# Optimization experiments

Hardware: AMD Instinct MI355X
Metric: run time of the kernel (lower is better)

The kernel has to match this reference:

```python
import jax, jax.numpy as jnp
import numpy as np

N = 100000       # num_nodes
E = 1600000      # num_edges (avg degree 16)
EL = 200000      # link-prediction edges
IN_C = 64
POS = 16
HID = 64
OUT = 32


def setup_inputs() -> dict:
    key = jax.random.key(0)
    ks = jax.random.split(key, 10)
    def glorot(k, shape):
        scale = 1.0 / np.sqrt(shape[0])
        return jax.random.uniform(k, shape, jnp.float32, -scale, scale)
    return {
        "x": jax.random.normal(ks[0], (N, IN_C), jnp.float32),
        "pos_emb": jax.random.normal(ks[1], (N, POS), jnp.float32),
        "W1": glorot(ks[2], (IN_C + POS, HID)),
        "b1": jnp.zeros((HID,), jnp.float32),
        "W2": glorot(ks[3], (HID, OUT)),
        "b2": jnp.zeros((OUT,), jnp.float32),
        "Wl": glorot(ks[4], (2 * OUT, 1)),
        "bl": jnp.zeros((1,), jnp.float32),
        "edge_index": jax.random.randint(ks[5], (2, E), 0, N, jnp.int32),
        "edge_label_index": jax.random.randint(ks[6], (2, EL), 0, N, jnp.int32),
    }


def reference(x, pos_emb, W1, b1, W2, b2, Wl, bl, edge_index, edge_label_index):
    n = x.shape[0]
    # GCNConv: add self-loops, symmetric deg^{-1/2} normalization (PyG defaults)
    loops = jnp.arange(n, dtype=edge_index.dtype)
    src = jnp.concatenate([edge_index[0], loops])  # [E+N]
    dst = jnp.concatenate([edge_index[1], loops])  # [E+N]
    deg = jax.ops.segment_sum(jnp.ones_like(dst, jnp.float32), dst, num_segments=n)
    dinv = jnp.where(deg > 0, jax.lax.rsqrt(jnp.maximum(deg, 1e-12)), 0.0)
    norm = dinv[src] * dinv[dst]  # [E+N]

    def gcn_conv(h, W, b):
        hw = h @ W                                    # [N, d_out] transform first
        msg = hw[src] * norm[:, None]                 # gather + normalize
        return jax.ops.segment_sum(msg, dst, num_segments=n) + b  # scatter-add

    h = jnp.concatenate([x, pos_emb], axis=1)         # [N, in+pos]
    h = jax.nn.relu(gcn_conv(h, W1, b1))              # dropout is eval no-op
    z = gcn_conv(h, W2, b2)                           # [N, out]

    s, d = edge_label_index[0], edge_label_index[1]
    zc = jnp.concatenate([z[s], z[d]], axis=1)        # [EL, 2*out]
    edge_pred = (zc @ Wl + bl)[:, 0]                  # [EL]
    return z, edge_pred
```

## Files before the change

kernel.cpp:

```cpp
#include <hip/hip_runtime.h>
#include <hip/hip_fp16.h>

#define NN 100000
#define NE 1600000
#define NEL 200000
#define TM 64
#define TM2 128

#define NBUCK 196
#define CAPB  10240
#define TPE   8192

__global__ void k_initcur(int* __restrict__ gcur) {
    int i = threadIdx.x;
    if (i < NBUCK) gcur[i] = i * CAPB;
}

__global__ __launch_bounds__(256) void k_part(const int* __restrict__ src,
                                              const int* __restrict__ dst,
                                              int* __restrict__ gcur,
                                              int* __restrict__ part) {
    __shared__ int hist[NBUCK];
    __shared__ int base[NBUCK];
    __shared__ int rk[NBUCK];
    int tid = threadIdx.x;
    for (int i = tid; i < NBUCK; i += 256) { hist[i] = 0; rk[i] = 0; }
    __syncthreads();
    int e0 = blockIdx.x * TPE;
    int e1 = min(e0 + TPE, NE);
    for (int e = e0 + tid; e < e1; e += 256)
        atomicAdd(&hist[dst[e] >> 9], 1);
    __syncthreads();
    for (int i = tid; i < NBUCK; i += 256)
        base[i] = atomicAdd(&gcur[i], hist[i]);
    __syncthreads();
    for (int e = e0 + tid; e < e1; e += 256) {
        int d = dst[e];
        int s = src[e];
        int b = d >> 9;
        int r = atomicAdd(&rk[b], 1);
        part[base[b] + r] = ((d & 511) << 17) | s;
    }
}

__global__ void k_bscan2(const int* __restrict__ gcur, int* __restrict__ bbase) {
    __shared__ int s[256];
    int t = threadIdx.x;
    int cnt = (t < NBUCK) ? (gcur[t] - t * CAPB) : 0;
    s[t] = cnt;
    __syncthreads();
    for (int st = 1; st < 256; st <<= 1) {
        int tmp = (t >= st) ? s[t - st] : 0;
        __syncthreads();
        s[t] += tmp;
        __syncthreads();
    }
    if (t < NBUCK) bbase[t] = s[t] - cnt;
}

__global__ __launch_bounds__(256) void k_build(const int* __restrict__ gcur,
                                               const int* __restrict__ bbase,
                                               const int* __restrict__ part,
                                               int* __restrict__ csr,
                                               int* __restrict__ off,
                                               float* __restrict__ dinv) {
    __shared__ int hist[512];
    __shared__ int loff[512];
    __shared__ int ssum[256];
    __shared__ int csrbuf[CAPB];
    int b = blockIdx.x;
    int tid = threadIdx.x;
    int cnt = gcur[b] - b * CAPB;
    int pbase = b * CAPB;
    int obase = bbase[b];
    hist[tid] = 0; hist[tid + 256] = 0;
    __syncthreads();
    for (int i = tid; i < cnt; i += 256)
        atomicAdd(&hist[part[pbase + i] >> 17], 1);
    __syncthreads();
    int a0 = hist[2 * tid], a1 = hist[2 * tid + 1];
    int pairs = a0 + a1;
    ssum[tid] = pairs;
    __syncthreads();
    for (int st = 1; st < 256; st <<= 1) {
        int tmp = (tid >= st) ? ssum[tid - st] : 0;
        __syncthreads();
        ssum[tid] += tmp;
        __syncthreads();
    }
    int pexcl = ssum[tid] - pairs;
    loff[2 * tid] = pexcl;
    loff[2 * tid + 1] = pexcl + a0;
    __syncthreads();
    for (int i = tid; i < 512; i += 256) {
        int d = b * 512 + i;
        if (d < NN) {
            int c = hist[i];
            off[d] = obase + loff[i] + c;
            dinv[d] = rsqrtf((float)(c + 1));
        }
    }
    hist[tid] = 0; hist[tid + 256] = 0;
    __syncthreads();
    for (int i = tid; i < cnt; i += 256) {
        int rec = part[pbase + i];
        int dl = rec >> 17;
        int r = atomicAdd(&hist[dl], 1);
        csrbuf[loff[dl] + r] = rec & 0x1FFFF;
    }
    __syncthreads();
    for (int i = tid; i < cnt; i += 256)
        csr[obase + i] = csrbuf[i];
}

__global__ __launch_bounds__(256) void k_hw1(const float* __restrict__ x,
                                             const float* __restrict__ pos,
                                             const float* __restrict__ W1,
                                             const float* __restrict__ dinv,
                                             __half* __restrict__ hw1) {
    __shared__ float sh[TM * 80];
    __shared__ float sw[80 * 64];
    int tid = threadIdx.x;
    for (int t = tid; t < 80 * 64; t += 256) sw[t] = W1[t];
    int nb = blockIdx.x * TM;
    for (int i = tid; i < TM * 64; i += 256) {
        int node = i >> 6, ch = i & 63;
        int g = nb + node;
        sh[node * 80 + ch] = (g < NN) ? x[g * 64 + ch] : 0.0f;
    }
    for (int i = tid; i < TM * 16; i += 256) {
        int node = i >> 4, ch = i & 15;
        int g = nb + node;
        sh[node * 80 + 64 + ch] = (g < NN) ? pos[g * 16 + ch] : 0.0f;
    }
    __syncthreads();
    int j  = (tid & 15) * 4;
    int nl = (tid >> 4) * 4;
    float a00=0,a01=0,a02=0,a03=0, a10=0,a11=0,a12=0,a13=0;
    float a20=0,a21=0,a22=0,a23=0, a30=0,a31=0,a32=0,a33=0;
#pragma unroll 4
    for (int k = 0; k < 80; ++k) {
        float4 wv = *(const float4*)&sw[k * 64 + j];
        float h0 = sh[(nl + 0) * 80 + k];
        float h1 = sh[(nl + 1) * 80 + k];
        float h2 = sh[(nl + 2) * 80 + k];
        float h3 = sh[(nl + 3) * 80 + k];
        a00 += h0 * wv.x; a01 += h0 * wv.y; a02 += h0 * wv.z; a03 += h0 * wv.w;
        a10 += h1 * wv.x; a11 += h1 * wv.y; a12 += h1 * wv.z; a13 += h1 * wv.w;
        a20 += h2 * wv.x; a21 += h2 * wv.y; a22 += h2 * wv.z; a23 += h2 * wv.w;
        a30 += h3 * wv.x; a31 += h3 * wv.y; a32 += h3 * wv.z; a33 += h3 * wv.w;
    }
    int g0 = nb + nl;
    union { __half2 h2v[2]; float2 f2; } u;
#define STORE_ROW(r, b0, b1, b2, b3)                                          \
    if (g0 + r < NN) {                                                        \
        float sc = dinv[g0 + r];                                              \
        u.h2v[0] = __floats2half2_rn(b0 * sc, b1 * sc);                       \
        u.h2v[1] = __floats2half2_rn(b2 * sc, b3 * sc);                       \
        *(float2*)&hw1[(g0 + r) * 64 + j] = u.f2;                             \
    }
    STORE_ROW(0, a00, a01, a02, a03)
    STORE_ROW(1, a10, a11, a12, a13)
    STORE_ROW(2, a20, a21, a22, a23)
    STORE_ROW(3, a30, a31, a32, a33)
#undef STORE_ROW
}

__global__ __launch_bounds__(256) void k_gather1(const int* __restrict__ off,
                                                 const int* __restrict__ csr,
                                                 const float* __restrict__ dinv,
                                                 const __half* __restrict__ hw,
                                                 const float* __restrict__ b1,
                                                 __half* __restrict__ h2out) {
    int lane = threadIdx.x & 63;
    int wave = threadIdx.x >> 6;
    int d = blockIdx.x * 4 + wave;
    int start = (d == 0) ? 0 : off[d - 1];
    int end = off[d];
    start = __builtin_amdgcn_readfirstlane(start);
    end   = __builtin_amdgcn_readfirstlane(end);
    float dd = dinv[d];
    float hself = __half2float(hw[d * 64 + lane]);
    float acc0 = 0.0f, acc1 = 0.0f, acc2 = 0.0f, acc3 = 0.0f;
    int e = start;
    for (; e + 7 < end; e += 8) {
        int s0 = csr[e],     s1 = csr[e + 1];
        int s2 = csr[e + 2], s3 = csr[e + 3];
        int s4 = csr[e + 4], s5 = csr[e + 5];
        int s6 = csr[e + 6], s7 = csr[e + 7];
        float g0 = __half2float(hw[s0 * 64 + lane]);
        float g1 = __half2float(hw[s1 * 64 + lane]);
        float g2 = __half2float(hw[s2 * 64 + lane]);
        float g3 = __half2float(hw[s3 * 64 + lane]);
        float g4 = __half2float(hw[s4 * 64 + lane]);
        float g5 = __half2float(hw[s5 * 64 + lane]);
        float g6 = __half2float(hw[s6 * 64 + lane]);
        float g7 = __half2float(hw[s7 * 64 + lane]);
        acc0 += g0; acc1 += g1; acc2 += g2; acc3 += g3;
        acc0 += g4; acc1 += g5; acc2 += g6; acc3 += g7;
    }
    for (; e < end; ++e)
        acc0 += __half2float(hw[csr[e] * 64 + lane]);
    float v = fmaxf(b1[lane] + dd * (((acc0 + acc1) + (acc2 + acc3)) + hself), 0.0f);
    h2out[d * 64 + lane] = __float2half_rn(v);
}

__global__ __launch_bounds__(256) void k_hw2(const __half* __restrict__ h2,
                                             const float* __restrict__ W2,
                                             const float* __restrict__ dinv,
                                             __half* __restrict__ hw2) {
    __shared__ float sh[TM2 * 65];
    __shared__ float sw[64 * 32];
    int tid = threadIdx.x;
    for (int t = tid; t < 64 * 32; t += 256) sw[t] = W2[t];
    int nb = blockIdx.x * TM2;
    for (int i = tid; i < TM2 * 64; i += 256) {
        int node = i >> 6, ch = i & 63;
        int g = nb + node;
        sh[node * 65 + ch] = (g < NN) ? __half2float(h2[g * 64 + ch]) : 0.0f;
    }
    __syncthreads();
    int j  = (tid & 7) * 4;
    int nl = (tid >> 3) * 4;
    float a00=0,a01=0,a02=0,a03=0, a10=0,a11=0,a12=0,a13=0;
    float a20=0,a21=0,a22=0,a23=0, a30=0,a31=0,a32=0,a33=0;
#pragma unroll 4
    for (int k = 0; k < 64; ++k) {
        float4 wv = *(const float4*)&sw[k * 32 + j];
        float h0 = sh[(nl + 0) * 65 + k];
        float h1 = sh[(nl + 1) * 65 + k];
        float h2v = sh[(nl + 2) * 65 + k];
        float h3 = sh[(nl + 3) * 65 + k];
        a00 += h0 * wv.x;  a01 += h0 * wv.y;  a02 += h0 * wv.z;  a03 += h0 * wv.w;
        a10 += h1 * wv.x;  a11 += h1 * wv.y;  a12 += h1 * wv.z;  a13 += h1 * wv.w;
        a20 += h2v * wv.x; a21 += h2v * wv.y; a22 += h2v * wv.z; a23 += h2v * wv.w;
        a30 += h3 * wv.x;  a31 += h3 * wv.y;  a32 += h3 * wv.z;  a33 += h3 * wv.w;
    }
    int g0 = nb + nl;
    union { __half2 h2v2[2]; float2 f2; } u;
#define STORE_ROW(r, b0, b1, b2, b3)                                          \
    if (g0 + r < NN) {                                                        \
        float sc = dinv[g0 + r];                                              \
        u.h2v2[0] = __floats2half2_rn(b0 * sc, b1 * sc);                      \
        u.h2v2[1] = __floats2half2_rn(b2 * sc, b3 * sc);                      \
        *(float2*)&hw2[(g0 + r) * 32 + j] = u.f2;                             \
    }
    STORE_ROW(0, a00, a01, a02, a03)
    STORE_ROW(1, a10, a11, a12, a13)
    STORE_ROW(2, a20, a21, a22, a23)
    STORE_ROW(3, a30, a31, a32, a33)
#undef STORE_ROW
}

__global__ __launch_bounds__(256) void k_gather2(const int* __restrict__ off,
                                                 const int* __restrict__ csr,
                                                 const float* __restrict__ dinv,
                                                 const __half* __restrict__ hw,
                                                 const float* __restrict__ b2,
                                                 float* __restrict__ outz) {
    int lane = threadIdx.x & 63;
    int half = lane >> 5;
    int j = lane & 31;
    int wave = threadIdx.x >> 6;
    int d = blockIdx.x * 4 + wave;
    int start = (d == 0) ? 0 : off[d - 1];
    int end = off[d];
    start = __builtin_amdgcn_readfirstlane(start);
    end   = __builtin_amdgcn_readfirstlane(end);
    float dd = dinv[d];
    float hself = __half2float(hw[d * 32 + j]);
    float accA = 0.0f, accB = 0.0f, accC = 0.0f, accD = 0.0f;
    int e = start;
    for (; e + 7 < end; e += 8) {
        int sA = csr[e + half];
        int sB = csr[e + half + 2];
        int sC = csr[e + half + 4];
        int sD = csr[e + half + 6];
        accA += __half2float(hw[sA * 32 + j]);
        accB += __half2float(hw[sB * 32 + j]);
        accC += __half2float(hw[sC * 32 + j]);
        accD += __half2float(hw[sD * 32 + j]);
    }
    for (int ee = e + half; ee < end; ee += 2)
        accA += __half2float(hw[csr[ee] * 32 + j]);
    float acc = (accA + accB) + (accC + accD);
    acc += __shfl(acc, lane ^ 32, 64);
    if (half == 0)
        outz[d * 32 + j] = b2[j] + dd * (acc + hself);
}

__global__ __launch_bounds__(256) void k_linkpred(const int* __restrict__ sidx,
                                                  const int* __restrict__ didx,
                                                  const float* __restrict__ z,
                                                  const float* __restrict__ Wl,
                                                  const float* __restrict__ bl,
                                                  float* __restrict__ pred) {
    int t = blockIdx.x * blockDim.x + threadIdx.x;
    int e = t >> 4;
    int l = t & 15;
    int s = sidx[e], d = didx[e];
    float2 zs = *(const float2*)&z[s * 32 + 2 * l];
    float2 zd = *(const float2*)&z[d * 32 + 2 * l];
    float2 ws = *(const float2*)&Wl[2 * l];
    float2 wd = *(const float2*)&Wl[32 + 2 * l];
    float v = zs.x * ws.x + zs.y * ws.y + zd.x * wd.x + zd.y * wd.y;
    v += __shfl_xor(v, 1, 64);
    v += __shfl_xor(v, 2, 64);
    v += __shfl_xor(v, 4, 64);
    v += __shfl_xor(v, 8, 64);
    if (l == 0) pred[e] = v + bl[0];
}

extern "C" void kernel_launch(void* const* d_in, const int* in_sizes, int n_in,
                              void* d_out, int out_size, void* d_ws, size_t ws_size,
                              hipStream_t stream) {
    const float* x    = (const float*)d_in[0];
    const float* pos  = (const float*)d_in[1];
    const float* W1   = (const float*)d_in[2];
    const float* b1   = (const float*)d_in[3];
    const float* W2   = (const float*)d_in[4];
    const float* b2   = (const float*)d_in[5];
    const float* Wl   = (const float*)d_in[6];
    const float* bl   = (const float*)d_in[7];
    const int*   ei   = (const int*)d_in[8];
    const int*   eli  = (const int*)d_in[9];
    const int* src  = ei;
    const int* dst  = ei + NE;
    const int* lsrc = eli;
    const int* ldst = eli + NEL;

    float* out_z    = (float*)d_out;
    float* out_pred = (float*)d_out + NN * 32;

    float*  dinv  = (float*)d_ws;
    int*    off   = (int*)(dinv + NN);
    int*    gcur  = off + NN;
    int*    bbase = gcur + NBUCK;
    int*    csr   = bbase + NBUCK;
    __half* hw1   = (__half*)(csr + NE);
    int*    part  = (int*)hw1;
    __half* h2    = hw1 + NN * 64;
    __half* hw2   = h2 + NN * 64;

    k_initcur<<<1, 256, 0, stream>>>(gcur);
    k_part<<<(NE + TPE - 1) / TPE, 256, 0, stream>>>(src, dst, gcur, part);
    k_bscan2<<<1, 256, 0, stream>>>(gcur, bbase);
    k_build<<<NBUCK, 256, 0, stream>>>(gcur, bbase, part, csr, off, dinv);

    k_hw1<<<(NN + TM - 1) / TM, 256, 0, stream>>>(x, pos, W1, dinv, hw1);

    k_gather1<<<NN / 4, 256, 0, stream>>>(off, csr, dinv, hw1, b1, h2);

    k_hw2<<<(NN + TM2 - 1) / TM2, 256, 0, stream>>>(h2, W2, dinv, hw2);

    k_gather2<<<NN / 4, 256, 0, stream>>>(off, csr, dinv, hw2, b2, out_z);

    k_linkpred<<<NEL * 16 / 256, 256, 0, stream>>>(lsrc, ldst, out_z, Wl, bl, out_pred);
}
```

Baseline: 309.5 us.

## Fuse second-layer transform into gather1 and merge bucket scan into build

The layer-2 weight multiply (h @ W2, scaled by dinv) now runs inside the layer-1 gather kernel. Each wave applies W2 to its freshly computed hidden row using wave shuffles and a shared-memory copy of W2, so the intermediate h2 array no longer goes to global memory and the separate k_hw2 launch is gone. On the preprocessing side, the init kernel becomes a memset and the bucket-offset scan is folded into every k_build block, removing two tiny launches. In exchange, every gather1 block loads W2 into shared memory and adds 32 shuffle-FMA steps per node, and each build block repeats a small scan.

Result: no change. 314.1 us (+1.5%).

```diff
diff --git a/kernel.cpp b/kernel.cpp
--- a/kernel.cpp
+++ b/kernel.cpp
@@ -5,16 +5,10 @@
 #define NE 1600000
 #define NEL 200000
 #define TM 64
-#define TM2 128
 
 #define NBUCK 196
 #define CAPB  10240
 #define TPE   8192
-
-__global__ void k_initcur(int* __restrict__ gcur) {
-    int i = threadIdx.x;
-    if (i < NBUCK) gcur[i] = i * CAPB;
-}
 
 __global__ __launch_bounds__(256) void k_part(const int* __restrict__ src,
                                               const int* __restrict__ dst,
@@ -32,7 +26,7 @@
         atomicAdd(&hist[dst[e] >> 9], 1);
     __syncthreads();
     for (int i = tid; i < NBUCK; i += 256)
-        base[i] = atomicAdd(&gcur[i], hist[i]);
+        base[i] = i * CAPB + atomicAdd(&gcur[i], hist[i]);
     __syncthreads();
     for (int e = e0 + tid; e < e1; e += 256) {
         int d = dst[e];
@@ -43,36 +37,29 @@
     }
 }
 
-__global__ void k_bscan2(const int* __restrict__ gcur, int* __restrict__ bbase) {
-    __shared__ int s[256];
-    int t = threadIdx.x;
-    int cnt = (t < NBUCK) ? (gcur[t] - t * CAPB) : 0;
-    s[t] = cnt;
-    __syncthreads();
-    for (int st = 1; st < 256; st <<= 1) {
-        int tmp = (t >= st) ? s[t - st] : 0;
-        __syncthreads();
-        s[t] += tmp;
-        __syncthreads();
-    }
-    if (t < NBUCK) bbase[t] = s[t] - cnt;
-}
-
 __global__ __launch_bounds__(256) void k_build(const int* __restrict__ gcur,
-                                               const int* __restrict__ bbase,
                                                const int* __restrict__ part,
                                                int* __restrict__ csr,
                                                int* __restrict__ off,
                                                float* __restrict__ dinv) {
+    __shared__ int cnts[256];
     __shared__ int hist[512];
     __shared__ int loff[512];
     __shared__ int ssum[256];
     __shared__ int csrbuf[CAPB];
     int b = blockIdx.x;
     int tid = threadIdx.x;
-    int cnt = gcur[b] - b * CAPB;
+    cnts[tid] = (tid < NBUCK) ? gcur[tid] : 0;
+    __syncthreads();
+    for (int st = 1; st < 256; st <<= 1) {
+        int tmp = (tid >= st) ? cnts[tid - st] : 0;
+        __syncthreads();
+        cnts[tid] += tmp;
+        __syncthreads();
+    }
+    int obase = (b == 0) ? 0 : cnts[b - 1];
+    int cnt = gcur[b];
     int pbase = b * CAPB;
-    int obase = bbase[b];
     hist[tid] = 0; hist[tid + 256] = 0;
     __syncthreads();
     for (int i = tid; i < cnt; i += 256)
@@ -171,7 +158,11 @@
                                                  const float* __restrict__ dinv,
                                                  const __half* __restrict__ hw,
                                                  const float* __restrict__ b1,
-                                                 __half* __restrict__ h2out) {
+                                                 const float* __restrict__ W2,
+                                                 __half* __restrict__ hw2out) {
+    __shared__ float w[64 * 32];
+    for (int t = threadIdx.x; t < 64 * 32; t += 256) w[t] = W2[t];
+    __syncthreads();
     int lane = threadIdx.x & 63;
     int wave = threadIdx.x >> 6;
     int d = blockIdx.x * 4 + wave;
@@ -202,54 +193,14 @@
     for (; e < end; ++e)
         acc0 += __half2float(hw[csr[e] * 64 + lane]);
     float v = fmaxf(b1[lane] + dd * (((acc0 + acc1) + (acc2 + acc3)) + hself), 0.0f);
-    h2out[d * 64 + lane] = __float2half_rn(v);
-}
-
-__global__ __launch_bounds__(256) void k_hw2(const __half* __restrict__ h2,
-                                             const float* __restrict__ W2,
-                                             const float* __restrict__ dinv,
-                                             __half* __restrict__ hw2) {
-    __shared__ float sh[TM2 * 65];
-    __shared__ float sw[64 * 32];
-    int tid = threadIdx.x;
-    for (int t = tid; t < 64 * 32; t += 256) sw[t] = W2[t];
-    int nb = blockIdx.x * TM2;
-    for (int i = tid; i < TM2 * 64; i += 256) {
-        int node = i >> 6, ch = i & 63;
-        int g = nb + node;
-        sh[node * 65 + ch] = (g < NN) ? __half2float(h2[g * 64 + ch]) : 0.0f;
-    }
-    __syncthreads();
-    int j  = (tid & 7) * 4;
-    int nl = (tid >> 3) * 4;
-    float a00=0,a01=0,a02=0,a03=0, a10=0,a11=0,a12=0,a13=0;
-    float a20=0,a21=0,a22=0,a23=0, a30=0,a31=0,a32=0,a33=0;
-#pragma unroll 4
-    for (int k = 0; k < 64; ++k) {
-        float4 wv = *(const float4*)&sw[k * 32 + j];
-        float h0 = sh[(nl + 0) * 65 + k];
-        float h1 = sh[(nl + 1) * 65 + k];
-        float h2v = sh[(nl + 2) * 65 + k];
-        float h3 = sh[(nl + 3) * 65 + k];
-        a00 += h0 * wv.x;  a01 += h0 * wv.y;  a02 += h0 * wv.z;  a03 += h0 * wv.w;
-        a10 += h1 * wv.x;  a11 += h1 * wv.y;  a12 += h1 * wv.z;  a13 += h1 * wv.w;
-        a20 += h2v * wv.x; a21 += h2v * wv.y; a22 += h2v * wv.z; a23 += h2v * wv.w;
-        a30 += h3 * wv.x;  a31 += h3 * wv.y;  a32 += h3 * wv.z;  a33 += h3 * wv.w;
-    }
-    int g0 = nb + nl;
-    union { __half2 h2v2[2]; float2 f2; } u;
-#define STORE_ROW(r, b0, b1, b2, b3)                                          \
-    if (g0 + r < NN) {                                                        \
-        float sc = dinv[g0 + r];                                              \
-        u.h2v2[0] = __floats2half2_rn(b0 * sc, b1 * sc);                      \
-        u.h2v2[1] = __floats2half2_rn(b2 * sc, b3 * sc);                      \
-        *(float2*)&hw2[(g0 + r) * 32 + j] = u.f2;                             \
-    }
-    STORE_ROW(0, a00, a01, a02, a03)
-    STORE_ROW(1, a10, a11, a12, a13)
-    STORE_ROW(2, a20, a21, a22, a23)
-    STORE_ROW(3, a30, a31, a32, a33)
-#undef STORE_ROW
+    int j = lane & 31;
+    int base2 = (lane >> 5) << 5;
+    float acc = 0.0f;
+#pragma unroll 8
+    for (int k = 0; k < 32; ++k)
+        acc += __shfl(v, base2 + k, 64) * w[(base2 + k) * 32 + j];
+    acc += __shfl(acc, lane ^ 32, 64);
+    if (lane < 32) hw2out[d * 32 + j] = __float2half_rn(acc * dd);
 }
 
 __global__ __launch_bounds__(256) void k_gather2(const int* __restrict__ off,
@@ -335,23 +286,18 @@
     float*  dinv  = (float*)d_ws;
     int*    off   = (int*)(dinv + NN);
     int*    gcur  = off + NN;
-    int*    bbase = gcur + NBUCK;
-    int*    csr   = bbase + NBUCK;
+    int*    csr   = gcur + NBUCK;
     __half* hw1   = (__half*)(csr + NE);
     int*    part  = (int*)hw1;
-    __half* h2    = hw1 + NN * 64;
-    __half* hw2   = h2 + NN * 64;
-
-    k_initcur<<<1, 256, 0, stream>>>(gcur);
+    __half* hw2   = hw1 + NN * 64;
+
+    hipMemsetAsync(gcur, 0, NBUCK * sizeof(int), stream);
     k_part<<<(NE + TPE - 1) / TPE, 256, 0, stream>>>(src, dst, gcur, part);
-    k_bscan2<<<1, 256, 0, stream>>>(gcur, bbase);
-    k_build<<<NBUCK, 256, 0, stream>>>(gcur, bbase, part, csr, off, dinv);
+    k_build<<<NBUCK, 256, 0, stream>>>(gcur, part, csr, off, dinv);
 
     k_hw1<<<(NN + TM - 1) / TM, 256, 0, stream>>>(x, pos, W1, dinv, hw1);
 
-    k_gather1<<<NN / 4, 256, 0, stream>>>(off, csr, dinv, hw1, b1, h2);
-
-    k_hw2<<<(NN + TM2 - 1) / TM2, 256, 0, stream>>>(h2, W2, dinv, hw2);
+    k_gather1<<<NN / 4, 256, 0, stream>>>(off, csr, dinv, hw1, b1, W2, hw2);
 
     k_gather2<<<NN / 4, 256, 0, stream>>>(off, csr, dinv, hw2, b2, out_z);
 
```

## Split gather kernels by channel slice and fold bucket scan into build

Applied to the files above, without the earlier changes.

The gather kernels now assign each wave a 16-channel slice of a destination node, with four edge groups per wave reduced by shuffles. Blocks are interleaved so neighbouring blocks cover the other channel slices of the same nodes, which multiplies the block count. The separate bucket-scan and init kernels are removed: counts start from a memset and every build block redoes the prefix scan itself. This cuts launches, but the gathers become 32-bit-wide per-row reads with more redundant index loads and more waves.

Measured after the change: 459.8 us. +48.6%, slower.

```diff
diff --git a/kernel.cpp b/kernel.cpp
--- a/kernel.cpp
+++ b/kernel.cpp
@@ -10,11 +10,6 @@
 #define NBUCK 196
 #define CAPB  10240
 #define TPE   8192
-
-__global__ void k_initcur(int* __restrict__ gcur) {
-    int i = threadIdx.x;
-    if (i < NBUCK) gcur[i] = i * CAPB;
-}
 
 __global__ __launch_bounds__(256) void k_part(const int* __restrict__ src,
                                               const int* __restrict__ dst,
@@ -32,7 +27,7 @@
         atomicAdd(&hist[dst[e] >> 9], 1);
     __syncthreads();
     for (int i = tid; i < NBUCK; i += 256)
-        base[i] = atomicAdd(&gcur[i], hist[i]);
+        base[i] = i * CAPB + atomicAdd(&gcur[i], hist[i]);
     __syncthreads();
     for (int e = e0 + tid; e < e1; e += 256) {
         int d = dst[e];
@@ -43,36 +38,29 @@
     }
 }
 
-__global__ void k_bscan2(const int* __restrict__ gcur, int* __restrict__ bbase) {
-    __shared__ int s[256];
-    int t = threadIdx.x;
-    int cnt = (t < NBUCK) ? (gcur[t] - t * CAPB) : 0;
-    s[t] = cnt;
-    __syncthreads();
-    for (int st = 1; st < 256; st <<= 1) {
-        int tmp = (t >= st) ? s[t - st] : 0;
-        __syncthreads();
-        s[t] += tmp;
-        __syncthreads();
-    }
-    if (t < NBUCK) bbase[t] = s[t] - cnt;
-}
-
 __global__ __launch_bounds__(256) void k_build(const int* __restrict__ gcur,
-                                               const int* __restrict__ bbase,
                                                const int* __restrict__ part,
                                                int* __restrict__ csr,
                                                int* __restrict__ off,
                                                float* __restrict__ dinv) {
+    __shared__ int cnts[256];
     __shared__ int hist[512];
     __shared__ int loff[512];
     __shared__ int ssum[256];
     __shared__ int csrbuf[CAPB];
     int b = blockIdx.x;
     int tid = threadIdx.x;
-    int cnt = gcur[b] - b * CAPB;
+    cnts[tid] = (tid < NBUCK) ? gcur[tid] : 0;
+    __syncthreads();
+    for (int st = 1; st < 256; st <<= 1) {
+        int tmp = (tid >= st) ? cnts[tid - st] : 0;
+        __syncthreads();
+        cnts[tid] += tmp;
+        __syncthreads();
+    }
+    int obase = (b == 0) ? 0 : cnts[b - 1];
+    int cnt = gcur[b];
     int pbase = b * CAPB;
-    int obase = bbase[b];
     hist[tid] = 0; hist[tid + 256] = 0;
     __syncthreads();
     for (int i = tid; i < cnt; i += 256)
@@ -172,37 +160,37 @@
                                                  const __half* __restrict__ hw,
                                                  const float* __restrict__ b1,
                                                  __half* __restrict__ h2out) {
+    int g  = blockIdx.x & 7;
+    int q  = g >> 1;
+    int rb = (blockIdx.x >> 3) * 2 + (g & 1);
+    int wave = threadIdx.x >> 6;
     int lane = threadIdx.x & 63;
-    int wave = threadIdx.x >> 6;
-    int d = blockIdx.x * 4 + wave;
+    int d = rb * 4 + wave;
+    int eg = lane >> 4;
+    int ch = q * 16 + (lane & 15);
     int start = (d == 0) ? 0 : off[d - 1];
     int end = off[d];
     start = __builtin_amdgcn_readfirstlane(start);
     end   = __builtin_amdgcn_readfirstlane(end);
     float dd = dinv[d];
-    float hself = __half2float(hw[d * 64 + lane]);
-    float acc0 = 0.0f, acc1 = 0.0f, acc2 = 0.0f, acc3 = 0.0f;
+    float hself = __half2float(hw[d * 64 + ch]);
+    float acc0 = 0.0f, acc1 = 0.0f;
     int e = start;
     for (; e + 7 < end; e += 8) {
-        int s0 = csr[e],     s1 = csr[e + 1];
-        int s2 = csr[e + 2], s3 = csr[e + 3];
-        int s4 = csr[e + 4], s5 = csr[e + 5];
-        int s6 = csr[e + 6], s7 = csr[e + 7];
-        float g0 = __half2float(hw[s0 * 64 + lane]);
-        float g1 = __half2float(hw[s1 * 64 + lane]);
-        float g2 = __half2float(hw[s2 * 64 + lane]);
-        float g3 = __half2float(hw[s3 * 64 + lane]);
-        float g4 = __half2float(hw[s4 * 64 + lane]);
-        float g5 = __half2float(hw[s5 * 64 + lane]);
-        float g6 = __half2float(hw[s6 * 64 + lane]);
-        float g7 = __half2float(hw[s7 * 64 + lane]);
-        acc0 += g0; acc1 += g1; acc2 += g2; acc3 += g3;
-        acc0 += g4; acc1 += g5; acc2 += g6; acc3 += g7;
-    }
-    for (; e < end; ++e)
-        acc0 += __half2float(hw[csr[e] * 64 + lane]);
-    float v = fmaxf(b1[lane] + dd * (((acc0 + acc1) + (acc2 + acc3)) + hself), 0.0f);
-    h2out[d * 64 + lane] = __float2half_rn(v);
+        int sA = csr[e + eg];
+        int sB = csr[e + 4 + eg];
+        acc0 += __half2float(hw[sA * 64 + ch]);
+        acc1 += __half2float(hw[sB * 64 + ch]);
+    }
+    for (int ee = e + eg; ee < end; ee += 4)
+        acc0 += __half2float(hw[csr[ee] * 64 + ch]);
+    float acc = acc0 + acc1;
+    acc += __shfl_xor(acc, 16, 64);
+    acc += __shfl_xor(acc, 32, 64);
+    if (lane < 16) {
+        float v = fmaxf(b1[ch] + dd * (acc + hself), 0.0f);
+        h2out[d * 64 + ch] = __float2half_rn(v);
+    }
 }
 
 __global__ __launch_bounds__(256) void k_hw2(const __half* __restrict__ h2,
@@ -258,35 +246,35 @@
                                                  const __half* __restrict__ hw,
                                                  const float* __restrict__ b2,
                                                  float* __restrict__ outz) {
+    int g  = blockIdx.x & 7;
+    int h  = g >> 2;
+    int rb = (blockIdx.x >> 3) * 4 + (g & 3);
+    int wave = threadIdx.x >> 6;
     int lane = threadIdx.x & 63;
-    int half = lane >> 5;
-    int j = lane & 31;
-    int wave = threadIdx.x >> 6;
-    int d = blockIdx.x * 4 + wave;
+    int d = rb * 4 + wave;
+    int eg = lane >> 4;
+    int ch = h * 16 + (lane & 15);
     int start = (d == 0) ? 0 : off[d - 1];
     int end = off[d];
     start = __builtin_amdgcn_readfirstlane(start);
     end   = __builtin_amdgcn_readfirstlane(end);
     float dd = dinv[d];
-    float hself = __half2float(hw[d * 32 + j]);
-    float accA = 0.0f, accB = 0.0f, accC = 0.0f, accD = 0.0f;
+    float hself = __half2float(hw[d * 32 + ch]);
+    float acc0 = 0.0f, acc1 = 0.0f;
     int e = start;
     for (; e + 7 < end; e += 8) {
-        int sA = csr[e + half];
-        int sB = csr[e + half + 2];
-        int sC = csr[e + half + 4];
-        int sD = csr[e + half + 6];
-        accA += __half2float(hw[sA * 32 + j]);
-        accB += __half2float(hw[sB * 32 + j]);
-        accC += __half2float(hw[sC * 32 + j]);
-        accD += __half2float(hw[sD * 32 + j]);
-    }
-    for (int ee = e + half; ee < end; ee += 2)
-        accA += __half2float(hw[csr[ee] * 32 + j]);
-    float acc = (accA + accB) + (accC + accD);
-    acc += __shfl(acc, lane ^ 32, 64);
-    if (half == 0)
-        outz[d * 32 + j] = b2[j] + dd * (acc + hself);
+        int sA = csr[e + eg];
+        int sB = csr[e + 4 + eg];
+        acc0 += __half2float(hw[sA * 32 + ch]);
+        acc1 += __half2float(hw[sB * 32 + ch]);
+    }
+    for (int ee = e + eg; ee < end; ee += 4)
+        acc0 += __half2float(hw[csr[ee] * 32 + ch]);
+    float acc = acc0 + acc1;
+    acc += __shfl_xor(acc, 16, 64);
+    acc += __shfl_xor(acc, 32, 64);
+    if (lane < 16)
+        outz[d * 32 + ch] = b2[ch] + dd * (acc + hself);
 }
 
 __global__ __launch_bounds__(256) void k_linkpred(const int* __restrict__ sidx,
@@ -335,25 +323,23 @@
     float*  dinv  = (float*)d_ws;
     int*    off   = (int*)(dinv + NN);
     int*    gcur  = off + NN;
-    int*    bbase = gcur + NBUCK;
-    int*    csr   = bbase + NBUCK;
+    int*    csr   = gcur + NBUCK;
     __half* hw1   = (__half*)(csr + NE);
     int*    part  = (int*)hw1;
     __half* h2    = hw1 + NN * 64;
     __half* hw2   = h2 + NN * 64;
 
-    k_initcur<<<1, 256, 0, stream>>>(gcur);
+    hipMemsetAsync(gcur, 0, NBUCK * sizeof(int), stream);
     k_part<<<(NE + TPE - 1) / TPE, 256, 0, stream>>>(src, dst, gcur, part);
-    k_bscan2<<<1, 256, 0, stream>>>(gcur, bbase);
-    k_build<<<NBUCK, 256, 0, stream>>>(gcur, bbase, part, csr, off, dinv);
+    k_build<<<NBUCK, 256, 0, stream>>>(gcur, part, csr, off, dinv);
 
     k_hw1<<<(NN + TM - 1) / TM, 256, 0, stream>>>(x, pos, W1, dinv, hw1);
 
-    k_gather1<<<NN / 4, 256, 0, stream>>>(off, csr, dinv, hw1, b1, h2);
+    k_gather1<<<NN, 256, 0, stream>>>(off, csr, dinv, hw1, b1, h2);
 
     k_hw2<<<(NN + TM2 - 1) / TM2, 256, 0, stream>>>(h2, W2, dinv, hw2);
 
-    k_gather2<<<NN / 4, 256, 0, stream>>>(off, csr, dinv, hw2, b2, out_z);
+    k_gather2<<<NN / 2, 256, 0, stream>>>(off, csr, dinv, hw2, b2, out_z);
 
     k_linkpred<<<NEL * 16 / 256, 256, 0, stream>>>(lsrc, ldst, out_z, Wl, bl, out_pred);
 }
```
